# Optimization experiments

Measured on AMD Instinct MI355X. Metric: run time of the kernel, lower is better.

The kernel has to match this reference:

```python
import jax, jax.numpy as jnp
import numpy as np

B, L, D = 2, 2048, 512
NUM_HEADS = 8
LN_EPS = 1e-5


def setup_inputs() -> dict:
    key = jax.random.key(0)
    ks = jax.random.split(key, 4)
    s = 1.0 / np.sqrt(D)
    return {
        "x": jax.random.normal(ks[0], (B, L, D), dtype=jnp.float32),
        "in_proj_w": jax.random.normal(ks[1], (3 * D, D), dtype=jnp.float32) * s,
        "in_proj_b": jnp.zeros((3 * D,), dtype=jnp.float32),
        "out_proj_w": jax.random.normal(ks[2], (D, D), dtype=jnp.float32) * s,
        "out_proj_b": jnp.zeros((D,), dtype=jnp.float32),
        "ln_gamma": jnp.ones((D,), dtype=jnp.float32),
        "ln_beta": jnp.zeros((D,), dtype=jnp.float32),
        "window_size": 10,
    }


def reference(x, in_proj_w, in_proj_b, out_proj_w, out_proj_b, ln_gamma, ln_beta, window_size):
    b, l, d = x.shape
    h = NUM_HEADS
    hd = d // h

    # packed qkv projection (torch Linear: y = x @ W.T + b)
    qkv = x @ in_proj_w.T + in_proj_b  # [B, L, 3D]
    q, k, v = jnp.split(qkv, 3, axis=-1)

    def heads(t):  # [B, L, D] -> [B, H, L, hd]
        return t.reshape(b, l, h, hd).transpose(0, 2, 1, 3)

    q, k, v = heads(q), heads(k), heads(v)
    q = q * (1.0 / np.sqrt(hd))  # torch MHA scales q

    scores = jnp.einsum("bhqd,bhkd->bhqk", q, k)  # [B, H, L, L]

    # Faithful to the source + torch bool attn_mask semantics:
    # mask starts all-True, positions OUTSIDE window set to False;
    # torch masks (=-inf) where the bool mask is True, i.e. INSIDE
    # the window [i - w//2, i + w//2).
    half = window_size // 2
    i = jnp.arange(l)[:, None]
    j = jnp.arange(l)[None, :]
    banned = (j >= i - half) & (j < i + half)  # [L, L] bool
    scores = jnp.where(banned[None, None], -jnp.inf, scores)

    attn = jax.nn.softmax(scores, axis=-1)
    ctx = jnp.einsum("bhqk,bhkd->bhqd", attn, v)  # [B, H, L, hd]
    ctx = ctx.transpose(0, 2, 1, 3).reshape(b, l, d)
    attn_out = ctx @ out_proj_w.T + out_proj_b

    # residual + LayerNorm
    y = x + attn_out
    mu = jnp.mean(y, axis=-1, keepdims=True)
    var = jnp.mean(jnp.square(y - mu), axis=-1, keepdims=True)
    return (y - mu) * jax.lax.rsqrt(var + LN_EPS) * ln_gamma + ln_beta
```

## Files before the change

kernel.cpp:

```cpp
#include <hip/hip_runtime.h>
#include <hip/hip_bf16.h>
#include <math.h>

namespace {

constexpr int Bb = 2, Ll = 2048, Dd = 512, Hh = 8;
constexpr int M = Bb * Ll;
constexpr int THREE_D = 3 * Dd;

typedef __attribute__((ext_vector_type(8))) short short8;
typedef __attribute__((ext_vector_type(4))) short short4v;
typedef __attribute__((ext_vector_type(4))) float f32x4;

__device__ __forceinline__ unsigned short f2bf(float x) {
  union { __hip_bfloat16 h; unsigned short u; } cv;
  cv.h = __float2bfloat16(x);
  return cv.u;
}

__device__ __forceinline__ float fexp2(float x) {
  float r;
  asm("v_exp_f32 %0, %1" : "=v"(r) : "v"(x));
  return r;
}

__device__ __forceinline__ void gload_lds16(const void* g, void* l) {
  __builtin_amdgcn_global_load_lds(
      (const __attribute__((address_space(1))) void*)g,
      (__attribute__((address_space(3))) void*)l, 16, 0, 0);
}

constexpr int QUADS_X = (M * Dd) / 4;
constexpr int QUADS_W1 = (THREE_D * Dd) / 4;
constexpr int QUADS_W2 = (Dd * Dd) / 4;
constexpr int QUADS_TOT = QUADS_X + QUADS_W1 + QUADS_W2;

__global__ __launch_bounds__(256) void cvt_bf16(
    const float* __restrict__ x, const float* __restrict__ w1,
    const float* __restrict__ w2, unsigned short* __restrict__ xb,
    unsigned short* __restrict__ wb, unsigned short* __restrict__ wob) {
  const int i = blockIdx.x * 256 + threadIdx.x;
  const float* src;
  unsigned short* dst;
  if (i < QUADS_X) {
    src = x + 4 * (size_t)i;
    dst = xb + 4 * (size_t)i;
  } else if (i < QUADS_X + QUADS_W1) {
    const int j = i - QUADS_X;
    src = w1 + 4 * (size_t)j;
    dst = wb + 4 * (size_t)j;
  } else {
    const int j = i - (QUADS_X + QUADS_W1);
    src = w2 + 4 * (size_t)j;
    dst = wob + 4 * (size_t)j;
  }
  float4 v = *reinterpret_cast<const float4*>(src);
  ushort4 o;
  o.x = f2bf(v.x); o.y = f2bf(v.y); o.z = f2bf(v.z); o.w = f2bf(v.w);
  *reinterpret_cast<ushort4*>(dst) = o;
}

template <int BM, int K, int N, bool QKV>
__global__ __launch_bounds__(256) void gemm_mfma(
    const unsigned short* __restrict__ A, const unsigned short* __restrict__ B,
    const float* __restrict__ bias, const float* __restrict__ R,
    unsigned short* __restrict__ Cb, float* __restrict__ Cf) {
  __shared__ unsigned short As[BM * 64];
  __shared__ unsigned short Bs[128 * 64];
  constexpr int MF = BM / 32;
  constexpr int AL = BM / 32;

  const int tid = threadIdx.x;
  const int lane = tid & 63;
  const int wu = __builtin_amdgcn_readfirstlane(tid >> 6);
  const int q = lane & 15;
  const int g = lane >> 4;
  const int wr = wu >> 1, wc = wu & 1;
  const int m0 = blockIdx.y * BM, n0 = blockIdx.x * 128;

  const int srow = lane >> 3;
  const int scol = 8 * ((lane & 7) ^ srow);
  const unsigned short* Ag = A + (size_t)(m0 + (BM / 4) * wu + srow) * K + scol;
  const unsigned short* Bg = B + (size_t)(n0 + 32 * wu + srow) * K + scol;
  char* AsW = (char*)As + wu * (BM / 4) * 128;
  char* BsW = (char*)Bs + wu * 4096;

  f32x4 acc[MF][4] = {};

  for (int k0 = 0; k0 < K; k0 += 64) {
    __syncthreads();
#pragma unroll
    for (int i = 0; i < AL; ++i)
      gload_lds16(Ag + (size_t)(8 * i) * K + k0, AsW + 1024 * i);
#pragma unroll
    for (int i = 0; i < 4; ++i)
      gload_lds16(Bg + (size_t)(8 * i) * K + k0, BsW + 1024 * i);
    __syncthreads();

    const char* Abase = (const char*)As + (wr * (BM / 2) + q) * 128;
    const char* Bbase = (const char*)Bs + (wc * 64 + q) * 128;
#pragma unroll
    for (int s = 0; s < 2; ++s) {
      const int csw = (64 * s + 16 * g) ^ ((q & 7) << 4);
      short8 af[MF], bf[4];
#pragma unroll
      for (int m = 0; m < MF; ++m)
        af[m] = *reinterpret_cast<const short8*>(Abase + m * 2048 + csw);
#pragma unroll
      for (int n = 0; n < 4; ++n)
        bf[n] = *reinterpret_cast<const short8*>(Bbase + n * 2048 + csw);
#pragma unroll
      for (int m = 0; m < MF; ++m)
#pragma unroll
        for (int n = 0; n < 4; ++n)
          acc[m][n] = __builtin_amdgcn_mfma_f32_16x16x32_bf16(
              af[m], bf[n], acc[m][n], 0, 0, 0);
    }
  }

  const float sc = (QKV && n0 < Dd) ? 0.125f * 1.44269504f : 1.0f;
#pragma unroll
  for (int m = 0; m < MF; ++m) {
#pragma unroll
    for (int r = 0; r < 4; ++r) {
      const int row = m0 + wr * (BM / 2) + m * 16 + 4 * g + r;
#pragma unroll
      for (int n = 0; n < 4; ++n) {
        const int col = n0 + wc * 64 + n * 16 + q;
        const float v = acc[m][n][r] + bias[col];
        if (QKV) {
          Cb[(size_t)row * N + col] = f2bf(v * sc);
        } else {
          Cf[(size_t)row * N + col] = v + R[(size_t)row * N + col];
        }
      }
    }
  }
}

__global__ __launch_bounds__(512) void attn_mfma(
    const unsigned short* __restrict__ qkv, const int* __restrict__ wsz,
    unsigned short* __restrict__ ctx) {
  __shared__ unsigned short Kls[16384];
  __shared__ unsigned short Vls[16384];
  __shared__ unsigned short Pls[8192];

  const int tid = threadIdx.x;
  const int lane = tid & 63;
  const int w = tid >> 6;
  const int wu = __builtin_amdgcn_readfirstlane(w);
  const int wg = wu & 3;
  const int hv = wu >> 2;
  const int q = lane & 15;
  const int g = lane >> 4;

  const int qt = blockIdx.x & 31;
  const int h = (blockIdx.x >> 5) & 7;
  const int b = blockIdx.x >> 8;
  const int qbase = qt * 64;
  const int hwin = wsz[0] >> 1;

  const size_t bh_base = (size_t)b * Ll * THREE_D + h * 64;

  const unsigned short* qrow =
      qkv + bh_base + (size_t)(qbase + wg * 16 + q) * THREE_D;
  short8 qf0 = *reinterpret_cast<const short8*>(qrow + 8 * g);
  short8 qf1 = *reinterpret_cast<const short8*>(qrow + 32 + 8 * g);
  asm volatile("s_waitcnt vmcnt(0)" : "+v"(qf0), "+v"(qf1)::"memory");

  const int k_rowoff = wg * 16 + (lane >> 3);
  const int k_dcol = 8 * ((lane & 7) ^ ((lane >> 3) & 7));
  const unsigned short* kg_base = qkv + bh_base + Dd + k_dcol;

  const int v_rowoff = 32 * (wg >> 1) + 8 * ((lane >> 4) & 3) +
                       4 * ((lane >> 3) & 1) + ((lane >> 1) & 3);
  const unsigned short* vg_base = qkv + bh_base + 2 * Dd + 8 * (lane & 1);

  unsigned short* kst = &Kls[hv * 8192 + wg * 1024];
  unsigned short* vst = &Vls[hv * 8192 + wg * 1024];
  unsigned short* pw = &Pls[wu * 1024];
  const char* kbytes = (const char*)Kls + hv * 16384;
  const char* vbytes = (const char*)Vls + hv * 16384;
  char* pb = (char*)pw;

  f32x4 oacc[4] = {};
  float m_run = -1e30f, lp = 0.f;

  const int qlo = qbase + wg * 16;
  const int iq = qlo + q;

  for (int t = 0; t < 8; ++t) {
    const int kbase = hv * 1024 + t * 128;
    __syncthreads();

#pragma unroll
    for (int u = 0; u < 2; ++u) {
      const int kb = kbase + u * 64;
      gload_lds16(kg_base + (size_t)(kb + k_rowoff) * THREE_D, kst + u * 4096);
      gload_lds16(kg_base + (size_t)(kb + k_rowoff + 8) * THREE_D,
                  kst + u * 4096 + 512);
      gload_lds16(vg_base + (size_t)(kb + v_rowoff) * THREE_D +
                      16 * ((2 * wg + 0) & 3), vst + u * 4096);
      gload_lds16(vg_base + (size_t)(kb + v_rowoff) * THREE_D +
                      16 * ((2 * wg + 1) & 3), vst + u * 4096 + 512);
    }
    __syncthreads();

    f32x4 sa[8] = {};
    __builtin_amdgcn_s_setprio(1);
#pragma unroll
    for (int s = 0; s < 2; ++s) {
      const short8 qf = s ? qf1 : qf0;
#pragma unroll
      for (int n = 0; n < 8; ++n) {
        const int u = n >> 2, nn = n & 3;
        const int baddr =
            u * 8192 + ((((16 * nn + q) * 128 + 64 * s + 16 * g)) ^
                        ((q & 7) << 4));
        const short8 kf = *reinterpret_cast<const short8*>(kbytes + baddr);
        sa[n] = __builtin_amdgcn_mfma_f32_16x16x32_bf16(kf, qf, sa[n], 0, 0, 0);
      }
    }
    __builtin_amdgcn_s_setprio(0);

    if (kbase + 128 > qlo - hwin && kbase < qlo + 15 + hwin) {
#pragma unroll
      for (int n = 0; n < 8; ++n) {
#pragma unroll
        for (int r = 0; r < 4; ++r) {
          const int j = kbase + 16 * n + 4 * g + r;
          if (j >= iq - hwin && j < iq + hwin) sa[n][r] = -1e30f;
        }
      }
    }

    float mxa[8];
#pragma unroll
    for (int n = 0; n < 8; ++n)
      mxa[n] = fmaxf(fmaxf(fmaxf(sa[n][0], sa[n][1]), sa[n][2]), sa[n][3]);
    float mx = fmaxf(
        fmaxf(fmaxf(mxa[0], mxa[1]), fmaxf(mxa[2], mxa[3])),
        fmaxf(fmaxf(mxa[4], mxa[5]), fmaxf(mxa[6], mxa[7])));
    mx = fmaxf(mx, __shfl_xor(mx, 16));
    mx = fmaxf(mx, __shfl_xor(mx, 32));

    if (!__all(mx <= m_run + 8.0f)) {
      const float mnew = fmaxf(m_run, mx);
      const float corr = fexp2(m_run - mnew);
      m_run = mnew;
      lp *= corr;
      float corr_o[4];
#pragma unroll
      for (int r = 0; r < 4; ++r) corr_o[r] = __shfl(corr, 4 * g + r, 16);
#pragma unroll
      for (int n = 0; n < 4; ++n)
#pragma unroll
        for (int r = 0; r < 4; ++r) oacc[n][r] *= corr_o[r];
    }

#pragma unroll
    for (int n = 0; n < 8; ++n)
#pragma unroll
      for (int r = 0; r < 4; ++r) sa[n][r] = fexp2(sa[n][r] - m_run);
#pragma unroll
    for (int n = 0; n < 8; ++n)
      lp += (sa[n][0] + sa[n][1]) + (sa[n][2] + sa[n][3]);

#pragma unroll
    for (int u = 0; u < 2; ++u) {
#pragma unroll
      for (int n = 0; n < 4; ++n) {
        const f32x4 sv = sa[4 * u + n];
        uint2 pk;
        pk.x = (unsigned)f2bf(sv[0]) | ((unsigned)f2bf(sv[1]) << 16);
        pk.y = (unsigned)f2bf(sv[2]) | ((unsigned)f2bf(sv[3]) << 16);
        *reinterpret_cast<uint2*>(
            pb + q * 128 + ((32 * n + 8 * g) ^ ((q & 7) << 4))) = pk;
      }
      asm volatile("s_waitcnt lgkmcnt(0)" ::: "memory");

#pragma unroll
      for (int s = 0; s < 2; ++s) {
        const short8 pf = *reinterpret_cast<const short8*>(
            pb + q * 128 + ((64 * s + 16 * g) ^ ((q & 7) << 4)));
        short4v vlo[4], vhi[4];
#pragma unroll
        for (int n = 0; n < 4; ++n) {
          const __attribute__((address_space(3))) unsigned short* va =
              (const __attribute__((address_space(3))) unsigned short*)(
                  vbytes + u * 8192 + 4096 * s + 1024 * n + 256 * g + 8 * q);
          asm volatile("ds_read_b64_tr_b16 %0, %1 offset:0" : "=v"(vlo[n]) : "v"(va));
          asm volatile("ds_read_b64_tr_b16 %0, %1 offset:128" : "=v"(vhi[n]) : "v"(va));
        }
        asm volatile("s_waitcnt lgkmcnt(0)"
                     : "+v"(vlo[0]), "+v"(vhi[0]), "+v"(vlo[1]), "+v"(vhi[1]),
                       "+v"(vlo[2]), "+v"(vhi[2]), "+v"(vlo[3]), "+v"(vhi[3])
                     :
                     : "memory");
        __builtin_amdgcn_sched_barrier(0);
        __builtin_amdgcn_s_setprio(1);
#pragma unroll
        for (int n = 0; n < 4; ++n) {
          const short8 vf = __builtin_shufflevector(vlo[n], vhi[n], 0, 1, 2, 3,
                                                    4, 5, 6, 7);
          oacc[n] =
              __builtin_amdgcn_mfma_f32_16x16x32_bf16(pf, vf, oacc[n], 0, 0, 0);
        }
        __builtin_amdgcn_s_setprio(0);
      }
    }
  }

  lp += __shfl_xor(lp, 16);
  lp += __shfl_xor(lp, 32);
  const float l_run = lp;

  float* Om = (float*)Kls;
  float* mls = (float*)Vls;

  __syncthreads();
  if (w >= 4) {
#pragma unroll
    for (int r = 0; r < 4; ++r) {
      const int rr = wg * 16 + 4 * g + r;
#pragma unroll
      for (int n = 0; n < 4; ++n) Om[rr * 64 + 16 * n + q] = oacc[n][r];
    }
    if (g == 0)
      *reinterpret_cast<float2*>(&mls[(wg * 16 + q) * 2]) =
          make_float2(m_run, l_run);
  }
  __syncthreads();
  if (w < 4) {
#pragma unroll
    for (int r = 0; r < 4; ++r) {
      const int rr = wg * 16 + 4 * g + r;
      const float m_own = __shfl(m_run, 4 * g + r, 16);
      const float l_own = __shfl(l_run, 4 * g + r, 16);
      const float2 ml2 = *reinterpret_cast<const float2*>(&mls[rr * 2]);
      const float ms = fmaxf(m_own, ml2.x);
      const float c1 = fexp2(m_own - ms);
      const float c2 = fexp2(ml2.x - ms);
      const float inv = 1.0f / (c1 * l_own + c2 * ml2.y);
      const int row = qbase + rr;
      unsigned short* crow = ctx + ((size_t)(b * Ll + row)) * Dd + h * 64 + q;
#pragma unroll
      for (int n = 0; n < 4; ++n) {
        const float o2 = Om[rr * 64 + 16 * n + q];
        crow[16 * n] = f2bf((c1 * oacc[n][r] + c2 * o2) * inv);
      }
    }
  }
}

__global__ __launch_bounds__(256) void ln_kernel(
    const float* __restrict__ y, const float* __restrict__ gamma,
    const float* __restrict__ beta, float* __restrict__ out) {
  const int row = blockIdx.x;
  const int tid = threadIdx.x;
  const float* yr = y + (size_t)row * Dd;

  float2 v = *reinterpret_cast<const float2*>(&yr[tid * 2]);
  float s = v.x + v.y;
  float qq = v.x * v.x + v.y * v.y;
#pragma unroll
  for (int off = 1; off < 64; off <<= 1) {
    s += __shfl_xor(s, off, 64);
    qq += __shfl_xor(qq, off, 64);
  }
  __shared__ float ss[4], qs[4];
  if ((tid & 63) == 0) { ss[tid >> 6] = s; qs[tid >> 6] = qq; }
  __syncthreads();
  s = (ss[0] + ss[1]) + (ss[2] + ss[3]);
  qq = (qs[0] + qs[1]) + (qs[2] + qs[3]);

  const float mu = s * (1.0f / Dd);
  const float var = qq * (1.0f / Dd) - mu * mu;
  const float rstd = rsqrtf(var + 1e-5f);

  float2 gmv = *reinterpret_cast<const float2*>(&gamma[tid * 2]);
  float2 bev = *reinterpret_cast<const float2*>(&beta[tid * 2]);
  float2 o;
  o.x = (v.x - mu) * rstd * gmv.x + bev.x;
  o.y = (v.y - mu) * rstd * gmv.y + bev.y;
  *reinterpret_cast<float2*>(&out[(size_t)row * Dd + tid * 2]) = o;
}

}

extern "C" void kernel_launch(void* const* d_in, const int* in_sizes, int n_in,
                              void* d_out, int out_size, void* d_ws,
                              size_t ws_size, hipStream_t stream) {
  const float* x = (const float*)d_in[0];
  const float* w_in = (const float*)d_in[1];
  const float* b_in = (const float*)d_in[2];
  const float* w_out = (const float*)d_in[3];
  const float* b_out = (const float*)d_in[4];
  const float* gamma = (const float*)d_in[5];
  const float* beta = (const float*)d_in[6];
  const int* wsz = (const int*)d_in[7];
  float* out = (float*)d_out;

  unsigned short* ws16 = (unsigned short*)d_ws;
  unsigned short* qkvb = ws16;
  unsigned short* ctxb = ws16 + 6291456;
  unsigned short* xb = ws16 + 8388608;
  unsigned short* wb = ws16 + 10485760;
  unsigned short* wob = ws16 + 11272192;
  float* y = (float*)d_ws;

  dim3 blk(256);

  cvt_bf16<<<dim3(QUADS_TOT / 256), blk, 0, stream>>>(x, w_in, w_out, xb, wb,
                                                      wob);
  gemm_mfma<64, 512, 1536, true><<<dim3(12, 64), blk, 0, stream>>>(
      xb, wb, b_in, nullptr, qkvb, nullptr);
  attn_mfma<<<dim3(512), dim3(512), 0, stream>>>(qkvb, wsz, ctxb);
  gemm_mfma<64, 512, 512, false><<<dim3(4, 64), blk, 0, stream>>>(
      ctxb, wob, b_out, x, nullptr, y);
  ln_kernel<<<dim3(M), blk, 0, stream>>>(y, gamma, beta, out);
}
```

Baseline: 72.68 us.

## Fuse x fp32-to-bf16 conversion into QKV GEMM A-tile load; shrink out-proj tile

The QKV projection GEMM now reads x directly in fp32, converts each row chunk to bf16 in registers and writes it to swizzled LDS. This removes the bf16 copy of x and its conversion pass from the standalone cvt kernel. In exchange, the A-tile load becomes a synchronous register path instead of an async global-to-LDS load, and x is converted once per N-tile block, 12 times in all. The output projection also switches to BM=32 with twice as many blocks, for better occupancy.

```diff
diff --git a/kernel.cpp b/kernel.cpp
--- a/kernel.cpp
+++ b/kernel.cpp
@@ -30,27 +30,21 @@
       (__attribute__((address_space(3))) void*)l, 16, 0, 0);
 }
 
-constexpr int QUADS_X = (M * Dd) / 4;
 constexpr int QUADS_W1 = (THREE_D * Dd) / 4;
 constexpr int QUADS_W2 = (Dd * Dd) / 4;
-constexpr int QUADS_TOT = QUADS_X + QUADS_W1 + QUADS_W2;
+constexpr int QUADS_TOT = QUADS_W1 + QUADS_W2;
 
 __global__ __launch_bounds__(256) void cvt_bf16(
-    const float* __restrict__ x, const float* __restrict__ w1,
-    const float* __restrict__ w2, unsigned short* __restrict__ xb,
+    const float* __restrict__ w1, const float* __restrict__ w2,
     unsigned short* __restrict__ wb, unsigned short* __restrict__ wob) {
   const int i = blockIdx.x * 256 + threadIdx.x;
   const float* src;
   unsigned short* dst;
-  if (i < QUADS_X) {
-    src = x + 4 * (size_t)i;
-    dst = xb + 4 * (size_t)i;
-  } else if (i < QUADS_X + QUADS_W1) {
-    const int j = i - QUADS_X;
-    src = w1 + 4 * (size_t)j;
-    dst = wb + 4 * (size_t)j;
+  if (i < QUADS_W1) {
+    src = w1 + 4 * (size_t)i;
+    dst = wb + 4 * (size_t)i;
   } else {
-    const int j = i - (QUADS_X + QUADS_W1);
+    const int j = i - QUADS_W1;
     src = w2 + 4 * (size_t)j;
     dst = wob + 4 * (size_t)j;
   }
@@ -60,11 +54,12 @@
   *reinterpret_cast<ushort4*>(dst) = o;
 }
 
-template <int BM, int K, int N, bool QKV>
+template <int BM, int K, int N, int MODE>
 __global__ __launch_bounds__(256) void gemm_mfma(
-    const unsigned short* __restrict__ A, const unsigned short* __restrict__ B,
-    const float* __restrict__ bias, const float* __restrict__ R,
-    unsigned short* __restrict__ Cb, float* __restrict__ Cf) {
+    const unsigned short* __restrict__ A, const float* __restrict__ Af,
+    const unsigned short* __restrict__ B, const float* __restrict__ bias,
+    const float* __restrict__ R, unsigned short* __restrict__ Cb,
+    float* __restrict__ Cf) {
   __shared__ unsigned short As[BM * 64];
   __shared__ unsigned short Bs[128 * 64];
   constexpr int MF = BM / 32;
@@ -80,21 +75,46 @@
 
   const int srow = lane >> 3;
   const int scol = 8 * ((lane & 7) ^ srow);
-  const unsigned short* Ag = A + (size_t)(m0 + (BM / 4) * wu + srow) * K + scol;
   const unsigned short* Bg = B + (size_t)(n0 + 32 * wu + srow) * K + scol;
+  char* BsW = (char*)Bs + wu * 4096;
+
+  const unsigned short* Ag =
+      (MODE == 0) ? A + (size_t)(m0 + (BM / 4) * wu + srow) * K + scol
+                  : nullptr;
   char* AsW = (char*)As + wu * (BM / 4) * 128;
-  char* BsW = (char*)Bs + wu * 4096;
+
+  const float* Agf =
+      (MODE == 1)
+          ? Af + (size_t)(m0 + 16 * wu + (lane >> 3)) * K + 8 * (lane & 7)
+          : nullptr;
+  char* AsWb = (char*)As + (16 * wu + (lane >> 3)) * 128 +
+               16 * ((lane & 7) ^ (lane >> 3));
 
   f32x4 acc[MF][4] = {};
 
   for (int k0 = 0; k0 < K; k0 += 64) {
     __syncthreads();
 #pragma unroll
-    for (int i = 0; i < AL; ++i)
-      gload_lds16(Ag + (size_t)(8 * i) * K + k0, AsW + 1024 * i);
-#pragma unroll
     for (int i = 0; i < 4; ++i)
       gload_lds16(Bg + (size_t)(8 * i) * K + k0, BsW + 1024 * i);
+    if (MODE == 0) {
+#pragma unroll
+      for (int i = 0; i < AL; ++i)
+        gload_lds16(Ag + (size_t)(8 * i) * K + k0, AsW + 1024 * i);
+    } else {
+#pragma unroll
+      for (int hh = 0; hh < 2; ++hh) {
+        const float* ap = Agf + (size_t)(8 * hh) * K + k0;
+        float4 a0 = *reinterpret_cast<const float4*>(ap);
+        float4 a1 = *reinterpret_cast<const float4*>(ap + 4);
+        short8 pk;
+        pk[0] = (short)f2bf(a0.x); pk[1] = (short)f2bf(a0.y);
+        pk[2] = (short)f2bf(a0.z); pk[3] = (short)f2bf(a0.w);
+        pk[4] = (short)f2bf(a1.x); pk[5] = (short)f2bf(a1.y);
+        pk[6] = (short)f2bf(a1.z); pk[7] = (short)f2bf(a1.w);
+        *reinterpret_cast<short8*>(AsWb + 8 * hh * 128) = pk;
+      }
+    }
     __syncthreads();
 
     const char* Abase = (const char*)As + (wr * (BM / 2) + q) * 128;
@@ -118,7 +138,7 @@
     }
   }
 
-  const float sc = (QKV && n0 < Dd) ? 0.125f * 1.44269504f : 1.0f;
+  const float sc = (MODE == 1 && n0 < Dd) ? 0.125f * 1.44269504f : 1.0f;
 #pragma unroll
   for (int m = 0; m < MF; ++m) {
 #pragma unroll
@@ -128,7 +148,7 @@
       for (int n = 0; n < 4; ++n) {
         const int col = n0 + wc * 64 + n * 16 + q;
         const float v = acc[m][n][r] + bias[col];
-        if (QKV) {
+        if (MODE == 1) {
           Cb[(size_t)row * N + col] = f2bf(v * sc);
         } else {
           Cf[(size_t)row * N + col] = v + R[(size_t)row * N + col];
@@ -404,19 +424,17 @@
   unsigned short* ws16 = (unsigned short*)d_ws;
   unsigned short* qkvb = ws16;
   unsigned short* ctxb = ws16 + 6291456;
-  unsigned short* xb = ws16 + 8388608;
   unsigned short* wb = ws16 + 10485760;
   unsigned short* wob = ws16 + 11272192;
   float* y = (float*)d_ws;
 
   dim3 blk(256);
 
-  cvt_bf16<<<dim3(QUADS_TOT / 256), blk, 0, stream>>>(x, w_in, w_out, xb, wb,
-                                                      wob);
-  gemm_mfma<64, 512, 1536, true><<<dim3(12, 64), blk, 0, stream>>>(
-      xb, wb, b_in, nullptr, qkvb, nullptr);
+  cvt_bf16<<<dim3(QUADS_TOT / 256), blk, 0, stream>>>(w_in, w_out, wb, wob);
+  gemm_mfma<64, 512, 1536, 1><<<dim3(12, 64), blk, 0, stream>>>(
+      nullptr, x, wb, b_in, nullptr, qkvb, nullptr);
   attn_mfma<<<dim3(512), dim3(512), 0, stream>>>(qkvb, wsz, ctxb);
-  gemm_mfma<64, 512, 512, false><<<dim3(4, 64), blk, 0, stream>>>(
-      ctxb, wob, b_out, x, nullptr, y);
+  gemm_mfma<32, 512, 512, 0><<<dim3(4, 128), blk, 0, stream>>>(
+      ctxb, nullptr, wob, b_out, x, nullptr, y);
   ln_kernel<<<dim3(M), blk, 0, stream>>>(y, gamma, beta, out);
 }
```

New measurement: 75.28 us. 1.04x slower.
